# Kernel tuning notes

Measured on AMD Instinct MI355X. Metric: run time of the kernel, lower is better.

The kernel has to match this reference:

```python
import jax, jax.numpy as jnp
import numpy as np

B, S, H = 4, 2048, 1024

def setup_inputs() -> dict:
    key = jax.random.key(0)
    k = jax.random.split(key, 5)
    scale = 1.0 / np.sqrt(H)
    return {
        "hidden": jax.random.normal(k[0], (B, S, H), dtype=jnp.float32),
        "mask": jnp.zeros((B, 1, S, S), dtype=jnp.float32),
        "R": jax.random.normal(k[1], (S, S), dtype=jnp.float32),
        "G_w": jax.random.normal(k[2], (H, H), dtype=jnp.float32) * scale,
        "G_b": jnp.zeros((H,), dtype=jnp.float32),
        "F_w": jax.random.normal(k[3], (H, H), dtype=jnp.float32) * scale,
        "F_b": jnp.zeros((H,), dtype=jnp.float32),
    }

def reference(hidden, mask, R, G_w, G_b, F_w, F_b):
    # scores: [B, S, S] = learned random bias + additive attention mask
    scores = R + mask[:, 0]
    probs = jax.nn.softmax(scores, axis=-1)  # dropout is identity in eval mode
    values = jnp.einsum('bsh,oh->bso', hidden, G_w) + G_b  # G_linear
    out = jnp.einsum('bqk,bkh->bqh', probs, values)
    out = jnp.einsum('bsh,oh->bso', out, F_w) + F_b  # final_linear
    return out
```

## Files before the change

### kernel.cpp

```cpp
#include <hip/hip_runtime.h>
#include <hip/hip_bf16.h>

typedef __bf16 bf16x8 __attribute__((ext_vector_type(8)));
typedef __bf16 bf16x4 __attribute__((ext_vector_type(4)));
typedef float  f32x16 __attribute__((ext_vector_type(16)));

#define GPTR(p) ((__attribute__((address_space(1))) void*)(p))
#define LPTR(p) ((__attribute__((address_space(3))) void*)(p))

__global__ __launch_bounds__(256) void pre_kernel(
    const float* __restrict__ Fw, __bf16* __restrict__ f_bf,
    const float* __restrict__ Gw, __bf16* __restrict__ gt_bf,
    const float* __restrict__ Gb, const float* __restrict__ Fb,
    float* __restrict__ b2, int H) {
    __shared__ float tile[64][65];
    const int blk = blockIdx.x;
    const int t = threadIdx.x;

    if (blk < 512) {
        long i = ((long)blk * 256 + t) * 8;
        float4 a = *reinterpret_cast<const float4*>(Fw + i);
        float4 c = *reinterpret_cast<const float4*>(Fw + i + 4);
        bf16x8 o;
        o[0] = (__bf16)a.x; o[1] = (__bf16)a.y; o[2] = (__bf16)a.z; o[3] = (__bf16)a.w;
        o[4] = (__bf16)c.x; o[5] = (__bf16)c.y; o[6] = (__bf16)c.z; o[7] = (__bf16)c.w;
        *reinterpret_cast<bf16x8*>(f_bf + i) = o;
    } else if (blk < 768) {
        const int id = blk - 512;
        const int bx = (id & 15) * 64;
        const int by = (id >> 4) * 64;
        const int tr = t >> 4;
        const int tc = (t & 15) * 4;
#pragma unroll
        for (int i = 0; i < 4; i++) {
            float4 v = *reinterpret_cast<const float4*>(&Gw[(size_t)(by + tr + i * 16) * H + bx + tc]);
            tile[tr + i * 16][tc + 0] = v.x;
            tile[tr + i * 16][tc + 1] = v.y;
            tile[tr + i * 16][tc + 2] = v.z;
            tile[tr + i * 16][tc + 3] = v.w;
        }
        __syncthreads();
        const int wr = t >> 2;
        const int wc = (t & 3) * 16;
        bf16x8 o0, o1;
#pragma unroll
        for (int j = 0; j < 8; j++) o0[j] = (__bf16)tile[wc + j][wr];
#pragma unroll
        for (int j = 0; j < 8; j++) o1[j] = (__bf16)tile[wc + 8 + j][wr];
        *reinterpret_cast<bf16x8*>(&gt_bf[(size_t)(bx + wr) * H + by + wc]) = o0;
        *reinterpret_cast<bf16x8*>(&gt_bf[(size_t)(bx + wr) * H + by + wc + 8]) = o1;
    } else {
        const int o = blk - 768;
        float s = 0.f;
        for (int h = t; h < H; h += 256) s += Fw[(size_t)o * H + h] * Gb[h];
#pragma unroll
        for (int off = 32; off > 0; off >>= 1) s += __shfl_xor(s, off);
        __shared__ float ss[4];
        if ((t & 63) == 0) ss[t >> 6] = s;
        __syncthreads();
        if (t == 0) b2[o] = ss[0] + ss[1] + ss[2] + ss[3] + Fb[o];
    }
}

__global__ __launch_bounds__(256) void mid_kernel(
    const __bf16* __restrict__ f_bf, const __bf16* __restrict__ gt_bf,
    __bf16* __restrict__ Wm,
    const float* __restrict__ hidden, __bf16* __restrict__ xt,
    const float* __restrict__ R, const float* __restrict__ mask,
    __bf16* __restrict__ P, int H, int S) {
    const int blk = blockIdx.x;
    const int t = threadIdx.x;

    if (blk < 256) {
        __shared__ __bf16 As[64 * 64];
        __shared__ __bf16 Bs[64 * 64];
        const int lane = t & 63;
        const int wave = t >> 6;
        const int lane31 = lane & 31;
        const int hi = lane >> 5;
        const int wm = (wave >> 1) * 32;
        const int wn = (wave & 1) * 32;
        const int bm = (blk >> 4) * 64;
        const int bn = (blk & 15) * 64;

        const int rsub = lane >> 3;
        const int csub = lane & 7;
        const int lchunk = csub ^ rsub;
        const __bf16* ga0 = f_bf + (size_t)(bm + wave * 16 + rsub) * H + lchunk * 8;
        const __bf16* gb0 = gt_bf + (size_t)(bn + wave * 16 + rsub) * H + lchunk * 8;

        f32x16 acc = (f32x16)(0.f);
        for (int kt = 0; kt < H; kt += 64) {
            __syncthreads();
#pragma unroll
            for (int c = 0; c < 2; c++)
                __builtin_amdgcn_global_load_lds(GPTR(ga0 + (size_t)(c * 8) * H + kt),
                                                 LPTR(&As[(wave * 16 + c * 8) * 64]), 16, 0, 0);
#pragma unroll
            for (int c = 0; c < 2; c++)
                __builtin_amdgcn_global_load_lds(GPTR(gb0 + (size_t)(c * 8) * H + kt),
                                                 LPTR(&Bs[(wave * 16 + c * 8) * 64]), 16, 0, 0);
            __syncthreads();
#pragma unroll
            for (int s = 0; s < 4; s++) {
                const int ra = wm + lane31;
                const int rb = wn + lane31;
                bf16x8 af = *reinterpret_cast<const bf16x8*>(
                    &As[ra * 64 + (((2 * s + hi) ^ (ra & 7)) << 3)]);
                bf16x8 bfr = *reinterpret_cast<const bf16x8*>(
                    &Bs[rb * 64 + (((2 * s + hi) ^ (rb & 7)) << 3)]);
                acc = __builtin_amdgcn_mfma_f32_32x32x16_bf16(af, bfr, acc, 0, 0, 0);
            }
        }
        const int cm = bm + wm;
        const int cn = bn + wn + lane31;
#pragma unroll
        for (int rq = 0; rq < 4; rq++) {
            const int rbase = rq * 8 + 4 * hi;
#pragma unroll
            for (int rr = 0; rr < 4; rr++)
                Wm[(size_t)(cm + rbase + rr) * H + cn] = (__bf16)acc[rq * 4 + rr];
        }
    } else if (blk < 2304) {
        __shared__ float tile[64][65];
        const int id = blk - 256;
        const int b = id >> 9;
        const int tid = id & 511;
        const int by = (tid >> 4) * 64;
        const int bx = (tid & 15) * 64;
        const float* x = hidden + (size_t)b * S * H;
        __bf16* y = xt + (size_t)b * H * S;
        const int tr = t >> 4;
        const int tc = (t & 15) * 4;
#pragma unroll
        for (int i = 0; i < 4; i++) {
            float4 v = *reinterpret_cast<const float4*>(&x[(size_t)(by + tr + i * 16) * H + bx + tc]);
            tile[tr + i * 16][tc + 0] = v.x;
            tile[tr + i * 16][tc + 1] = v.y;
            tile[tr + i * 16][tc + 2] = v.z;
            tile[tr + i * 16][tc + 3] = v.w;
        }
        __syncthreads();
        const int wr = t >> 2;
        const int wc = (t & 3) * 16;
        bf16x8 o0, o1;
#pragma unroll
        for (int j = 0; j < 8; j++) o0[j] = (__bf16)tile[wc + j][wr];
#pragma unroll
        for (int j = 0; j < 8; j++) o1[j] = (__bf16)tile[wc + 8 + j][wr];
        *reinterpret_cast<bf16x8*>(&y[(size_t)(bx + wr) * S + by + wc]) = o0;
        *reinterpret_cast<bf16x8*>(&y[(size_t)(bx + wr) * S + by + wc + 8]) = o1;
    } else {
        const int id = blk - 2304;
        const int b = id >> 11;
        const int q = id & 2047;
        const int lane = t & 63, wave = t >> 6;
        const float* rrow = R + (size_t)q * S;
        const float* mrow = mask + ((size_t)b * S + q) * (size_t)S;
        __bf16* prow = P + ((size_t)b * S + q) * (size_t)S;

        float v[8];
#pragma unroll
        for (int i = 0; i < 2; i++) {
            float4 r4 = *reinterpret_cast<const float4*>(rrow + t * 8 + i * 4);
            float4 m4 = *reinterpret_cast<const float4*>(mrow + t * 8 + i * 4);
            v[i * 4 + 0] = r4.x + m4.x;
            v[i * 4 + 1] = r4.y + m4.y;
            v[i * 4 + 2] = r4.z + m4.z;
            v[i * 4 + 3] = r4.w + m4.w;
        }
        float mx = v[0];
#pragma unroll
        for (int i = 1; i < 8; i++) mx = fmaxf(mx, v[i]);
#pragma unroll
        for (int off = 32; off > 0; off >>= 1) mx = fmaxf(mx, __shfl_xor(mx, off));
        __shared__ float smax[4], ssum[4];
        if (lane == 0) smax[wave] = mx;
        __syncthreads();
        mx = fmaxf(fmaxf(smax[0], smax[1]), fmaxf(smax[2], smax[3]));
        float sum = 0.f;
#pragma unroll
        for (int i = 0; i < 8; i++) { v[i] = __expf(v[i] - mx); sum += v[i]; }
#pragma unroll
        for (int off = 32; off > 0; off >>= 1) sum += __shfl_xor(sum, off);
        if (lane == 0) ssum[wave] = sum;
        __syncthreads();
        sum = ssum[0] + ssum[1] + ssum[2] + ssum[3];
        const float inv = 1.0f / sum;
        bf16x8 o;
#pragma unroll
        for (int i = 0; i < 8; i++) o[i] = (__bf16)(v[i] * inv);
        *reinterpret_cast<bf16x8*>(prow + t * 8) = o;
    }
}

template <bool CFLOAT, bool BIAS, int SWZMODE>
__global__ __launch_bounds__(128) void gemm_nt_kernel(
    const __bf16* __restrict__ A, const __bf16* __restrict__ B,
    const float* __restrict__ bias, void* __restrict__ Cv,
    int K, int lda, int ldb, int ldc,
    long strideA, long strideB, long strideC) {
    const int t = threadIdx.x;
    const int lane = t & 63;
    const int wave = t >> 6;
    const int lane31 = lane & 31;
    const int hi = lane >> 5;
    int bm, bn, bz;
    if constexpr (SWZMODE == 1) {
        const int id = blockIdx.x;
        const int xcd = id & 7;
        const int slot = id >> 3;
        bz = xcd >> 1;
        bm = ((xcd & 1) * 16 + (slot >> 3)) * 64;
        bn = (slot & 7) * 128;
    } else if constexpr (SWZMODE == 2) {
        const int id = blockIdx.x;
        const int xcd = id & 7;
        const int slot = id >> 3;
        bz = 0;
        bm = (xcd * 16 + (slot >> 3)) * 64;
        bn = (slot & 7) * 128;
    } else {
        bm = blockIdx.y * 64;
        bn = blockIdx.x * 128;
        bz = blockIdx.z;
    }

    A += (size_t)bz * strideA;
    B += (size_t)bz * strideB;

    __shared__ __bf16 smem[12288];
    __bf16* const As = smem;
    __bf16* const Bs = smem + 4096;

    const int rsub = lane >> 3;
    const int csub = lane & 7;
    const int lchunk = csub ^ rsub;
    const __bf16* ga0 = A + (size_t)(bm + wave * 32 + rsub) * lda + lchunk * 8;
    const __bf16* gb0 = B + (size_t)(bn + wave * 64 + rsub) * ldb + lchunk * 8;

    f32x16 acc[2][2];
#pragma unroll
    for (int i = 0; i < 2; i++)
#pragma unroll
        for (int j = 0; j < 2; j++) acc[i][j] = (f32x16)(0.f);

    for (int kt = 0; kt < K; kt += 64) {
        __syncthreads();
#pragma unroll
        for (int c = 0; c < 4; c++)
            __builtin_amdgcn_global_load_lds(GPTR(ga0 + (size_t)(c * 8) * lda + kt),
                                             LPTR(&As[(wave * 32 + c * 8) * 64]), 16, 0, 0);
#pragma unroll
        for (int c = 0; c < 8; c++)
            __builtin_amdgcn_global_load_lds(GPTR(gb0 + (size_t)(c * 8) * ldb + kt),
                                             LPTR(&Bs[(wave * 64 + c * 8) * 64]), 16, 0, 0);
        __syncthreads();
#pragma unroll
        for (int s = 0; s < 4; s++) {
            bf16x8 af[2], bfr[2];
#pragma unroll
            for (int mi = 0; mi < 2; mi++) {
                const int r = mi * 32 + lane31;
                af[mi] = *reinterpret_cast<const bf16x8*>(
                    &As[r * 64 + (((2 * s + hi) ^ (r & 7)) << 3)]);
            }
#pragma unroll
            for (int ni = 0; ni < 2; ni++) {
                const int r = wave * 64 + ni * 32 + lane31;
                bfr[ni] = *reinterpret_cast<const bf16x8*>(
                    &Bs[r * 64 + (((2 * s + hi) ^ (r & 7)) << 3)]);
            }
#pragma unroll
            for (int mi = 0; mi < 2; mi++)
#pragma unroll
                for (int ni = 0; ni < 2; ni++)
                    acc[mi][ni] = __builtin_amdgcn_mfma_f32_32x32x16_bf16(af[mi], bfr[ni], acc[mi][ni], 0, 0, 0);
        }
    }

    __bf16* Cb = (__bf16*)Cv + (size_t)bz * strideC;
    float* Cf = (float*)Cv + (size_t)bz * strideC;
#pragma unroll
    for (int mi = 0; mi < 2; mi++)
#pragma unroll
        for (int ni = 0; ni < 2; ni++) {
            const int cm = bm + mi * 32;
            const int cn = bn + wave * 64 + ni * 32 + lane31;
            const float bv = BIAS ? bias[cn] : 0.0f;
#pragma unroll
            for (int rq = 0; rq < 4; rq++) {
                const int rbase = rq * 8 + 4 * hi;
                if constexpr (CFLOAT) {
#pragma unroll
                    for (int rr = 0; rr < 4; rr++)
                        Cf[(size_t)(cm + rbase + rr) * ldc + cn] = acc[mi][ni][rq * 4 + rr] + bv;
                } else {
#pragma unroll
                    for (int rr = 0; rr < 4; rr++)
                        Cb[(size_t)(cm + rbase + rr) * ldc + cn] = (__bf16)(acc[mi][ni][rq * 4 + rr] + bv);
                }
            }
        }
}

extern "C" void kernel_launch(void* const* d_in, const int* in_sizes, int n_in,
                              void* d_out, int out_size, void* d_ws, size_t ws_size,
                              hipStream_t stream) {
    const float* hidden = (const float*)d_in[0];
    const float* mask   = (const float*)d_in[1];
    const float* R      = (const float*)d_in[2];
    const float* G_w    = (const float*)d_in[3];
    const float* G_b    = (const float*)d_in[4];
    const float* F_w    = (const float*)d_in[5];
    const float* F_b    = (const float*)d_in[6];
    float* out = (float*)d_out;

    constexpr int B = 4, S = 2048, H = 1024;
    char* ws = (char*)d_ws;
    __bf16* xt    = (__bf16*)(ws);
    __bf16* t1    = (__bf16*)(ws + (16ll << 20));
    __bf16* probs = (__bf16*)(ws + (32ll << 20));
    __bf16* f_bf  = (__bf16*)(ws + (64ll << 20));
    __bf16* gt_bf = (__bf16*)(ws + (66ll << 20));
    __bf16* Wm    = (__bf16*)(ws + (68ll << 20));
    float*  b2    = (float*)(ws + (70ll << 20));

    pre_kernel<<<1792, 256, 0, stream>>>(F_w, f_bf, G_w, gt_bf, G_b, F_b, b2, H);

    mid_kernel<<<10496, 256, 0, stream>>>(f_bf, gt_bf, Wm, hidden, xt,
                                          R, mask, probs, H, S);

    gemm_nt_kernel<false, false, 1><<<1024, 128, 0, stream>>>(
        probs, xt, nullptr, t1, S, S, S, H,
        (long)S * S, (long)H * S, (long)S * H);

    gemm_nt_kernel<true, true, 2><<<1024, 128, 0, stream>>>(
        t1, Wm, b2, out, H, H, H, H, 0, 0, 0);
}
```

Baseline: 236.2 us.

## Enlarge GEMM tiles to 128x128 with four waves and double-buffered LDS

The GEMM kernel moves from 64x128 tiles with two waves to 128x128 tiles with four waves arranged 2x2, so each block reuses more data per load. It also double-buffers the LDS stages: the next K-tile is fetched with global_load_lds while the current one is consumed, leaving one barrier per iteration instead of two. Grids are halved to 512 blocks. LDS use rises to 64KB per block, which lowers occupancy, and with 512 blocks there may be too few blocks to fill all CUs. No wait on the async loads is added before the barrier, so correctness depends on the barrier covering the loads into LDS.

Result: faster. 225.4 us (-4.5%).

```diff
diff --git a/kernel.cpp b/kernel.cpp
--- a/kernel.cpp
+++ b/kernel.cpp
@@ -195,7 +195,7 @@
 }
 
 template <bool CFLOAT, bool BIAS, int SWZMODE>
-__global__ __launch_bounds__(128) void gemm_nt_kernel(
+__global__ __launch_bounds__(256) void gemm_nt_kernel(
     const __bf16* __restrict__ A, const __bf16* __restrict__ B,
     const float* __restrict__ bias, void* __restrict__ Cv,
     int K, int lda, int ldb, int ldc,
@@ -205,69 +205,74 @@
     const int wave = t >> 6;
     const int lane31 = lane & 31;
     const int hi = lane >> 5;
+    const int wm = (wave >> 1) * 64;
+    const int wn = (wave & 1) * 64;
     int bm, bn, bz;
     if constexpr (SWZMODE == 1) {
         const int id = blockIdx.x;
         const int xcd = id & 7;
         const int slot = id >> 3;
         bz = xcd >> 1;
-        bm = ((xcd & 1) * 16 + (slot >> 3)) * 64;
+        bm = ((xcd & 1) * 8 + (slot >> 3)) * 128;
         bn = (slot & 7) * 128;
-    } else if constexpr (SWZMODE == 2) {
+    } else {
         const int id = blockIdx.x;
         const int xcd = id & 7;
         const int slot = id >> 3;
         bz = 0;
-        bm = (xcd * 16 + (slot >> 3)) * 64;
+        bm = (xcd * 8 + (slot >> 3)) * 128;
         bn = (slot & 7) * 128;
-    } else {
-        bm = blockIdx.y * 64;
-        bn = blockIdx.x * 128;
-        bz = blockIdx.z;
     }
 
     A += (size_t)bz * strideA;
     B += (size_t)bz * strideB;
 
-    __shared__ __bf16 smem[12288];
-    __bf16* const As = smem;
-    __bf16* const Bs = smem + 4096;
+    __shared__ __bf16 smem[32768];
 
     const int rsub = lane >> 3;
     const int csub = lane & 7;
     const int lchunk = csub ^ rsub;
     const __bf16* ga0 = A + (size_t)(bm + wave * 32 + rsub) * lda + lchunk * 8;
-    const __bf16* gb0 = B + (size_t)(bn + wave * 64 + rsub) * ldb + lchunk * 8;
-
-    f32x16 acc[2][2];
-#pragma unroll
-    for (int i = 0; i < 2; i++)
-#pragma unroll
-        for (int j = 0; j < 2; j++) acc[i][j] = (f32x16)(0.f);
-
-    for (int kt = 0; kt < K; kt += 64) {
-        __syncthreads();
+    const __bf16* gb0 = B + (size_t)(bn + wave * 32 + rsub) * ldb + lchunk * 8;
+
+    auto stage = [&](int p, int kt) {
+        __bf16* As_ = smem + p * 16384;
+        __bf16* Bs_ = smem + p * 16384 + 8192;
 #pragma unroll
         for (int c = 0; c < 4; c++)
             __builtin_amdgcn_global_load_lds(GPTR(ga0 + (size_t)(c * 8) * lda + kt),
-                                             LPTR(&As[(wave * 32 + c * 8) * 64]), 16, 0, 0);
-#pragma unroll
-        for (int c = 0; c < 8; c++)
+                                             LPTR(&As_[(wave * 32 + c * 8) * 64]), 16, 0, 0);
+#pragma unroll
+        for (int c = 0; c < 4; c++)
             __builtin_amdgcn_global_load_lds(GPTR(gb0 + (size_t)(c * 8) * ldb + kt),
-                                             LPTR(&Bs[(wave * 64 + c * 8) * 64]), 16, 0, 0);
-        __syncthreads();
+                                             LPTR(&Bs_[(wave * 32 + c * 8) * 64]), 16, 0, 0);
+    };
+
+    f32x16 acc[2][2];
+#pragma unroll
+    for (int i = 0; i < 2; i++)
+#pragma unroll
+        for (int j = 0; j < 2; j++) acc[i][j] = (f32x16)(0.f);
+
+    stage(0, 0);
+    __syncthreads();
+    int p = 0;
+    for (int kt = 0; kt < K; kt += 64) {
+        if (kt + 64 < K) stage(p ^ 1, kt + 64);
+        const __bf16* As = smem + p * 16384;
+        const __bf16* Bs = smem + p * 16384 + 8192;
 #pragma unroll
         for (int s = 0; s < 4; s++) {
             bf16x8 af[2], bfr[2];
 #pragma unroll
             for (int mi = 0; mi < 2; mi++) {
-                const int r = mi * 32 + lane31;
+                const int r = wm + mi * 32 + lane31;
                 af[mi] = *reinterpret_cast<const bf16x8*>(
                     &As[r * 64 + (((2 * s + hi) ^ (r & 7)) << 3)]);
             }
 #pragma unroll
             for (int ni = 0; ni < 2; ni++) {
-                const int r = wave * 64 + ni * 32 + lane31;
+                const int r = wn + ni * 32 + lane31;
                 bfr[ni] = *reinterpret_cast<const bf16x8*>(
                     &Bs[r * 64 + (((2 * s + hi) ^ (r & 7)) << 3)]);
             }
@@ -277,6 +282,8 @@
                 for (int ni = 0; ni < 2; ni++)
                     acc[mi][ni] = __builtin_amdgcn_mfma_f32_32x32x16_bf16(af[mi], bfr[ni], acc[mi][ni], 0, 0, 0);
         }
+        __syncthreads();
+        p ^= 1;
     }
 
     __bf16* Cb = (__bf16*)Cv + (size_t)bz * strideC;
@@ -285,8 +292,8 @@
     for (int mi = 0; mi < 2; mi++)
 #pragma unroll
         for (int ni = 0; ni < 2; ni++) {
-            const int cm = bm + mi * 32;
-            const int cn = bn + wave * 64 + ni * 32 + lane31;
+            const int cm = bm + wm + mi * 32;
+            const int cn = bn + wn + ni * 32 + lane31;
             const float bv = BIAS ? bias[cn] : 0.0f;
 #pragma unroll
             for (int rq = 0; rq < 4; rq++) {
@@ -331,10 +338,10 @@
     mid_kernel<<<10496, 256, 0, stream>>>(f_bf, gt_bf, Wm, hidden, xt,
                                           R, mask, probs, H, S);
 
-    gemm_nt_kernel<false, false, 1><<<1024, 128, 0, stream>>>(
+    gemm_nt_kernel<false, false, 1><<<512, 256, 0, stream>>>(
         probs, xt, nullptr, t1, S, S, S, H,
         (long)S * S, (long)H * S, (long)S * H);
 
-    gemm_nt_kernel<true, true, 2><<<1024, 128, 0, stream>>>(
+    gemm_nt_kernel<true, true, 2><<<512, 256, 0, stream>>>(
         t1, Wm, b2, out, H, H, H, H, 0, 0, 0);
 }
```
